# Performance work log

Hardware: AMD Instinct MI355X
Metric: run time of the kernel (lower is better)

The kernel has to match this reference:

```python
import jax, jax.numpy as jnp
import numpy as np

# HeteNet distribute_compute reference: per-agent expert id (hete_pick) selects one of
# E heterogeneous expert MLPs; tokens are gathered per expert, run through that expert's
# actor net, and scattered back into a padded [n_threads, n_agents, n_action] output.
# Here each expert is a 2-layer MLP (Net._act actor head approximation):
#   logits = relu(x @ W1[e] + b1[e]) @ W2[e] + b2[e]
# The dispatch/combine is expressed as dense per-expert compute + one-hot combine,
# which is the mathematically identical (mask-select) form of the gather/scatter.

T, N, D, H, A, E = 64, 64, 512, 512, 32, 15  # threads, agents, obs_dim(+addon), hidden, actions, experts


def setup_inputs() -> dict:
    key = jax.random.key(0)
    k0, k1, k2, k3 = jax.random.split(key, 4)
    obs = jax.random.normal(k0, (T, N, D), dtype=jnp.float32)
    hete_pick = jax.random.randint(k1, (T, N), 0, E)  # expert id per agent
    W1 = jax.random.normal(k2, (E, D, H), dtype=jnp.float32) * (1.0 / np.sqrt(D))
    b1 = jnp.zeros((E, H), dtype=jnp.float32)
    W2 = jax.random.normal(k3, (E, H, A), dtype=jnp.float32) * (1.0 / np.sqrt(H))
    b2 = jnp.zeros((E, A), dtype=jnp.float32)
    return {"obs": obs, "W1": W1, "b1": b1, "W2": W2, "b2": b2, "hete_pick": hete_pick}


def reference(obs, W1, b1, W2, b2, hete_pick):
    # per-expert dense forward: [E, T, N, H]
    h = jax.nn.relu(jnp.einsum('tnd,edh->etnh', obs, W1) + b1[:, None, None, :])
    logits = jnp.einsum('etnh,eha->etna', h, W2) + b2[:, None, None, :]  # [E,T,N,A]
    # combine: scatter each expert's rows back per mask (hete_pick == e)
    onehot = (hete_pick[None, :, :] == jnp.arange(E)[:, None, None]).astype(obs.dtype)  # [E,T,N]
    return jnp.einsum('etna,etn->tna', logits, onehot)  # [T,N,A]
```

## Files before the change

kernel.cpp:

```cpp
#include <hip/hip_runtime.h>
#include <stdint.h>

#define NTOK 4096
#define DDIM 512
#define HDIM 512
#define ADIM 32
#define NEXP 15
#define TILE_M 64
#define GRID_M 160

typedef __attribute__((ext_vector_type(8))) short bf16x8;
typedef __attribute__((ext_vector_type(8))) unsigned short ushort8;
typedef __attribute__((ext_vector_type(4))) unsigned short ushort4v;
typedef __attribute__((ext_vector_type(4))) float f32x4;

__device__ __forceinline__ unsigned short f2bf(float f) {
  unsigned int u = __float_as_uint(f);
  u += 0x7fffu + ((u >> 16) & 1u);
  return (unsigned short)(u >> 16);
}

__device__ __forceinline__ void gld_lds16(const void* g, void* l) {
  __builtin_amdgcn_global_load_lds(
      (const __attribute__((address_space(1))) void*)g,
      (__attribute__((address_space(3))) void*)l, 16, 0, 0);
}

__global__ __launch_bounds__(256) void prep_kernel(
    const float* __restrict__ W1, const float* __restrict__ W2,
    const int* __restrict__ pick, int* __restrict__ meta,
    int* __restrict__ lists, unsigned short* __restrict__ W1I,
    unsigned short* __restrict__ W2T, float* __restrict__ out)
{
  extern __shared__ char smem[];
  const int bid = blockIdx.x;
  const int tid = threadIdx.x;
  if (bid < 240) {
    float* s = (float*)smem;
    const int e = bid / 16, kc = bid % 16, r0 = kc * 32;
    const float* src = W1 + (size_t)e * (DDIM * HDIM) + (size_t)r0 * HDIM;
    #pragma unroll
    for (int v = 0; v < 16; ++v) {
      int i = v * 256 + tid;
      int row = i >> 7, col = (i & 127) * 4;
      *(float4*)(s + row * 517 + col) = *(const float4*)(src + (size_t)row * 512 + col);
    }
    __syncthreads();
    unsigned short* dst = W1I + (size_t)(e * 16 + kc) * 512 * 32;
    const int p = tid & 3;
    #pragma unroll
    for (int w = 0; w < 8; ++w) {
      int n = w * 64 + (tid >> 2);
      int q = p ^ ((n >> 1) & 3);
      ushort8 vv;
      #pragma unroll
      for (int x = 0; x < 8; ++x) vv[x] = f2bf(s[(q * 8 + x) * 517 + n]);
      *(ushort8*)(dst + (size_t)n * 32 + p * 8) = vv;
    }
  } else if (bid < 255) {
    float4 z4; z4.x = 0.f; z4.y = 0.f; z4.z = 0.f; z4.w = 0.f;
    for (int i = (bid - 240) * 256 + tid; i < NTOK * ADIM / 4; i += 15 * 256)
      ((float4*)out)[i] = z4;
    float* s = (float*)smem;
    const int e = bid - 240;
    const float* src = W2 + (size_t)e * (HDIM * ADIM);
    #pragma unroll
    for (int v = 0; v < 16; ++v) {
      int i = v * 256 + tid;
      int row = i >> 3, col = (i & 7) * 4;
      *(float4*)(s + row * 36 + col) = *(const float4*)(src + (size_t)row * 32 + col);
    }
    __syncthreads();
    unsigned short* dst = W2T + (size_t)e * (ADIM * HDIM);
    const int a = tid >> 3, k0 = (tid & 7) * 64;
    #pragma unroll
    for (int w = 0; w < 8; ++w) {
      ushort8 vv;
      #pragma unroll
      for (int x = 0; x < 8; ++x) vv[x] = f2bf(s[(size_t)(k0 + w * 8 + x) * 36 + a]);
      *(ushort8*)(dst + (size_t)a * 512 + k0 + w * 8) = vv;
    }
  } else {
    int* s_inc = (int*)smem;
    int* s_run = s_inc + NEXP * 256;
    int pk[16];
    #pragma unroll
    for (int i = 0; i < 16; ++i) pk[i] = pick[tid * 16 + i];
    #pragma unroll
    for (int e = 0; e < NEXP; ++e) {
      int c = 0;
      #pragma unroll
      for (int i = 0; i < 16; ++i) c += (pk[i] == e) ? 1 : 0;
      s_inc[e * 256 + tid] = c;
    }
    __syncthreads();
    for (int off = 1; off < 256; off <<= 1) {
      int v[NEXP];
      #pragma unroll
      for (int e = 0; e < NEXP; ++e) v[e] = (tid >= off) ? s_inc[e * 256 + tid - off] : 0;
      __syncthreads();
      #pragma unroll
      for (int e = 0; e < NEXP; ++e) s_inc[e * 256 + tid] += v[e];
      __syncthreads();
    }
    #pragma unroll
    for (int e = 0; e < NEXP; ++e) s_run[e * 256 + tid] = (tid > 0) ? s_inc[e * 256 + tid - 1] : 0;
    __syncthreads();
    #pragma unroll
    for (int i = 0; i < 16; ++i) {
      int p = pk[i];
      int pos = s_run[p * 256 + tid]++;
      lists[p * NTOK + pos] = tid * 16 + i;
    }
    if (tid < NEXP) meta[tid] = s_inc[tid * 256 + 255];
    __syncthreads();
    if (tid == 0) {
      int tot = 0;
      for (int ee = 0; ee < NEXP; ++ee) {
        int c = s_inc[ee * 256 + 255];
        int nt = (c + TILE_M - 1) / TILE_M;
        for (int i = 0; i < nt; ++i) meta[16 + tot++] = (ee << 16) | i;
      }
      meta[15] = tot;
    }
  }
}

__global__ __launch_bounds__(256, 1) void moe_gemm(
    const float* __restrict__ obs, const float* __restrict__ b1,
    const float* __restrict__ b2, const int* __restrict__ meta,
    const int* __restrict__ lists, const unsigned short* __restrict__ W1I,
    const unsigned short* __restrict__ W2T, float* __restrict__ out)
{
  const int ntiles = meta[15];
  const int nphys = ntiles * 2;
  const int p = blockIdx.x;
  const int xq = nphys >> 3, xr = nphys & 7;
  const int xcd = p & 7, slot = p >> 3;
  const int cx = xq + (xcd < xr ? 1 : 0);
  if (slot >= cx) return;
  const int j2 = xcd * xq + (xcd < xr ? xcd : xr) + slot;
  const int jt = j2 >> 1, half = j2 & 1;

  const int tl = meta[16 + jt];
  const int e = tl >> 16;
  const int tile_lo = (tl & 0xffff) * TILE_M;
  const int cnt = meta[e];
  int mvalid = cnt - tile_lo; if (mvalid > TILE_M) mvalid = TILE_M;

  extern __shared__ char smem[];
  char* s_x = smem;
  char* wb0 = smem + 65536;
  char* wb1 = smem + 81920;
  char* wb2 = smem + 98304;

  const int tid = threadIdx.x, lane = tid & 63, wave = tid >> 6;
  const int l15 = lane & 15, l4 = lane >> 4;
  const int nbl = wave * 64;
  const int hbase = half * 256;
  const int* mylist = lists + e * NTOK;
  const unsigned short* w1i_e = W1I + (size_t)e * 16 * 512 * 32;
  const unsigned short* w2t_e = W2T + (size_t)e * (ADIM * HDIM);

  auto issue_w1 = [&](int t, char* buf) {
    const unsigned short* base = w1i_e + (size_t)t * (512 * 32) + (size_t)hbase * 32;
    #pragma unroll
    for (int i = 0; i < 4; ++i) {
      int nb = nbl + i * 16;
      gld_lds16(base + (size_t)nb * 32 + lane * 8, buf + nb * 64);
    }
  };
  issue_w1(0, wb0);
  __builtin_amdgcn_sched_barrier(0);
  issue_w1(1, wb1);
  __builtin_amdgcn_sched_barrier(0);

  {
    const int m = tid >> 2, sq = tid & 3;
    int idx = tile_lo + m; if (idx >= cnt) idx = cnt - 1;
    const float* grow = obs + (size_t)mylist[idx] * DDIM;
    #pragma unroll 4
    for (int si = 0; si < 16; ++si) {
      const int s = sq + si * 4;
      float4 f0 = *(const float4*)(grow + s * 8);
      float4 f1 = *(const float4*)(grow + s * 8 + 4);
      ushort8 v;
      v[0] = f2bf(f0.x); v[1] = f2bf(f0.y); v[2] = f2bf(f0.z); v[3] = f2bf(f0.w);
      v[4] = f2bf(f1.x); v[5] = f2bf(f1.y); v[6] = f2bf(f1.z); v[7] = f2bf(f1.w);
      *(ushort8*)(s_x + m * 1024 + ((s ^ (m & 7)) << 4)) = v;
    }
  }
  __syncthreads();

  f32x4 acc[4][4];
  #pragma unroll
  for (int nt = 0; nt < 4; ++nt) {
    float4 bv = *(const float4*)(b1 + e * HDIM + hbase + nbl + nt * 16 + l4 * 4);
    f32x4 b4 = {bv.x, bv.y, bv.z, bv.w};
    #pragma unroll
    for (int mt = 0; mt < 4; ++mt) acc[nt][mt] = b4;
  }

  #pragma unroll
  for (int t = 0; t < 16; ++t) {
    if (t < 14) {
      char* nxt = ((t + 2) % 3 == 0) ? wb0 : ((t + 2) % 3 == 1) ? wb1 : wb2;
      issue_w1(t + 2, nxt);
    } else if (t == 14) {
      #pragma unroll
      for (int i = 0; i < 4; ++i) {
        int o = wave * 4096 + i * 1024 + lane * 16;
        int a = o >> 9;
        int p16 = (o >> 4) & 31;
        gld_lds16(w2t_e + (size_t)a * 512 + hbase + (size_t)((p16 ^ (a & 7)) * 8),
                  wb1 + o);
      }
    }
    if (t < 15) asm volatile("s_waitcnt vmcnt(8)" ::: "memory");
    else        asm volatile("s_waitcnt vmcnt(4)" ::: "memory");
    __builtin_amdgcn_sched_barrier(0);

    const char* cw = (t % 3 == 0) ? wb0 : (t % 3 == 1) ? wb1 : wb2;
    bf16x8 wfr[4], xfr[4];
    #pragma unroll
    for (int nt = 0; nt < 4; ++nt) {
      int n = nbl + nt * 16 + l15;
      wfr[nt] = *(const bf16x8*)(cw + n * 64 + ((l4 ^ ((n >> 1) & 3)) << 4));
    }
    #pragma unroll
    for (int mt = 0; mt < 4; ++mt) {
      int mm = mt * 16 + l15;
      xfr[mt] = *(const bf16x8*)(s_x + mm * 1024 + ((((t << 2) + l4) ^ (mm & 7)) << 4));
    }
    #pragma unroll
    for (int nt = 0; nt < 4; ++nt)
      #pragma unroll
      for (int mt = 0; mt < 4; ++mt)
        acc[nt][mt] = __builtin_amdgcn_mfma_f32_16x16x32_bf16(wfr[nt], xfr[mt], acc[nt][mt], 0, 0, 0);
  }

  __syncthreads();

  #pragma unroll
  for (int nt = 0; nt < 4; ++nt) {
    int n0 = nbl + nt * 16 + l4 * 4;
    int sg = n0 >> 3, hsel = (n0 >> 2) & 1;
    #pragma unroll
    for (int mt = 0; mt < 4; ++mt) {
      int mm = mt * 16 + l15;
      ushort4v hv;
      #pragma unroll
      for (int r = 0; r < 4; ++r) hv[r] = f2bf(fmaxf(acc[nt][mt][r], 0.f));
      *(ushort4v*)(s_x + mm * 1024 + ((sg ^ (mm & 7)) << 4) + hsel * 8) = hv;
    }
  }
  __syncthreads();

  const int mm2 = wave * 16 + l15;
  f32x4 acc2[2];
  #pragma unroll
  for (int at = 0; at < 2; ++at) {
    float b2v = half ? 0.f : b2[e * ADIM + at * 16 + l15];
    f32x4 b4 = {b2v, b2v, b2v, b2v};
    acc2[at] = b4;
  }
  #pragma unroll
  for (int ks = 0; ks < 8; ++ks) {
    bf16x8 af = *(const bf16x8*)(s_x + mm2 * 1024 + ((((ks << 2) + l4) ^ (mm2 & 7)) << 4));
    #pragma unroll
    for (int at = 0; at < 2; ++at) {
      int a = at * 16 + l15;
      bf16x8 bf = *(const bf16x8*)(wb1 + a * 512 + ((((ks << 2) + l4) ^ (a & 7)) << 4));
      acc2[at] = __builtin_amdgcn_mfma_f32_16x16x32_bf16(af, bf, acc2[at], 0, 0, 0);
    }
  }
  #pragma unroll
  for (int at = 0; at < 2; ++at)
    #pragma unroll
    for (int r = 0; r < 4; ++r) {
      int mrow = wave * 16 + l4 * 4 + r;
      if (mrow < mvalid)
        atomicAdd(&out[(size_t)mylist[tile_lo + mrow] * ADIM + at * 16 + l15], acc2[at][r]);
    }
}

__global__ __launch_bounds__(256) void naive_kernel(
    const float* __restrict__ obs, const float* __restrict__ W1,
    const float* __restrict__ b1, const float* __restrict__ W2,
    const float* __restrict__ b2, const int* __restrict__ pick,
    float* __restrict__ out)
{
  __shared__ float sx[DDIM];
  __shared__ float sh[HDIM];
  const int t = blockIdx.x, tid = threadIdx.x;
  const int e = pick[t];
  const float* x = obs + (size_t)t * DDIM;
  for (int i = tid; i < DDIM; i += 256) sx[i] = x[i];
  __syncthreads();
  const float* w1 = W1 + (size_t)e * DDIM * HDIM;
  for (int j = tid; j < HDIM; j += 256) {
    float a = b1[e * HDIM + j];
    for (int d = 0; d < DDIM; ++d) a = fmaf(sx[d], w1[(size_t)d * HDIM + j], a);
    sh[j] = a > 0.f ? a : 0.f;
  }
  __syncthreads();
  if (tid < ADIM) {
    const float* w2 = W2 + (size_t)e * HDIM * ADIM;
    float a = b2[e * ADIM + tid];
    for (int j = 0; j < HDIM; ++j) a = fmaf(sh[j], w2[(size_t)j * ADIM + tid], a);
    out[(size_t)t * ADIM + tid] = a;
  }
}

extern "C" void kernel_launch(void* const* d_in, const int* in_sizes, int n_in,
                              void* d_out, int out_size, void* d_ws, size_t ws_size,
                              hipStream_t stream)
{
  const float* obs = (const float*)d_in[0];
  const float* W1  = (const float*)d_in[1];
  const float* b1  = (const float*)d_in[2];
  const float* W2  = (const float*)d_in[3];
  const float* b2  = (const float*)d_in[4];
  const int* pick  = (const int*)d_in[5];
  float* out = (float*)d_out;
  (void)in_sizes; (void)n_in; (void)out_size;

  const size_t OFF_LISTS = 1024;
  const size_t OFF_W1I   = 262144;
  const size_t OFF_W2T   = OFF_W1I + (size_t)NEXP * HDIM * DDIM * 2;
  const size_t WS_NEEDED = OFF_W2T + (size_t)NEXP * ADIM * HDIM * 2;

  if (ws_size < WS_NEEDED) {
    naive_kernel<<<dim3(NTOK), dim3(256), 0, stream>>>(obs, W1, b1, W2, b2, pick, out);
    return;
  }

  char* ws = (char*)d_ws;
  int* meta   = (int*)ws;
  int* lists  = (int*)(ws + OFF_LISTS);
  unsigned short* W1I = (unsigned short*)(ws + OFF_W1I);
  unsigned short* W2T = (unsigned short*)(ws + OFF_W2T);

  prep_kernel<<<dim3(256), dim3(256), 73728, stream>>>(
      W1, W2, pick, meta, lists, W1I, W2T, out);
  moe_gemm<<<dim3(GRID_M), dim3(256), 114688, stream>>>(
      obs, b1, b2, meta, lists, W1I, W2T, out);
}
```

Baseline: 28.57 us.

## Halve MoE token tile to 32 rows, raise occupancy, prefetch obs early

Shrinks the per-expert token tile from 64 to 32 rows, which roughly doubles the number of tiles and the grid size. It cuts shared memory so two blocks can share a CU, and loads the obs rows into registers before issuing the W1 prefetch so the two transfers overlap. The second GEMM is remapped so each wave handles one 16x16 output block. The cost is that every expert weight block is streamed twice as often, raising weight traffic, while padding waste in partially filled tiles goes down.

```diff
diff --git a/kernel.cpp b/kernel.cpp
--- a/kernel.cpp
+++ b/kernel.cpp
@@ -6,8 +6,8 @@
 #define HDIM 512
 #define ADIM 32
 #define NEXP 15
-#define TILE_M 64
-#define GRID_M 160
+#define TILE_M 32
+#define GRID_M 288
 
 typedef __attribute__((ext_vector_type(8))) short bf16x8;
 typedef __attribute__((ext_vector_type(8))) unsigned short ushort8;
@@ -126,7 +126,7 @@
   }
 }
 
-__global__ __launch_bounds__(256, 1) void moe_gemm(
+__global__ __launch_bounds__(256, 2) void moe_gemm(
     const float* __restrict__ obs, const float* __restrict__ b1,
     const float* __restrict__ b2, const int* __restrict__ meta,
     const int* __restrict__ lists, const unsigned short* __restrict__ W1I,
@@ -150,9 +150,9 @@
 
   extern __shared__ char smem[];
   char* s_x = smem;
-  char* wb0 = smem + 65536;
-  char* wb1 = smem + 81920;
-  char* wb2 = smem + 98304;
+  char* wb0 = smem + 32768;
+  char* wb1 = smem + 49152;
+  char* wb2 = smem + 65536;
 
   const int tid = threadIdx.x, lane = tid & 63, wave = tid >> 6;
   const int l15 = lane & 15, l4 = lane >> 4;
@@ -162,6 +162,17 @@
   const unsigned short* w1i_e = W1I + (size_t)e * 16 * 512 * 32;
   const unsigned short* w2t_e = W2T + (size_t)e * (ADIM * HDIM);
 
+  const int m = tid >> 3, s8 = tid & 7;
+  int idx = tile_lo + m; if (idx >= cnt) idx = cnt - 1;
+  const float* grow = obs + (size_t)mylist[idx] * DDIM;
+  float4 xf[16];
+  #pragma unroll
+  for (int si = 0; si < 8; ++si) {
+    xf[si * 2]     = *(const float4*)(grow + (s8 + si * 8) * 8);
+    xf[si * 2 + 1] = *(const float4*)(grow + (s8 + si * 8) * 8 + 4);
+  }
+  __builtin_amdgcn_sched_barrier(0);
+
   auto issue_w1 = [&](int t, char* buf) {
     const unsigned short* base = w1i_e + (size_t)t * (512 * 32) + (size_t)hbase * 32;
     #pragma unroll
@@ -175,30 +186,23 @@
   issue_w1(1, wb1);
   __builtin_amdgcn_sched_barrier(0);
 
-  {
-    const int m = tid >> 2, sq = tid & 3;
-    int idx = tile_lo + m; if (idx >= cnt) idx = cnt - 1;
-    const float* grow = obs + (size_t)mylist[idx] * DDIM;
-    #pragma unroll 4
-    for (int si = 0; si < 16; ++si) {
-      const int s = sq + si * 4;
-      float4 f0 = *(const float4*)(grow + s * 8);
-      float4 f1 = *(const float4*)(grow + s * 8 + 4);
-      ushort8 v;
-      v[0] = f2bf(f0.x); v[1] = f2bf(f0.y); v[2] = f2bf(f0.z); v[3] = f2bf(f0.w);
-      v[4] = f2bf(f1.x); v[5] = f2bf(f1.y); v[6] = f2bf(f1.z); v[7] = f2bf(f1.w);
-      *(ushort8*)(s_x + m * 1024 + ((s ^ (m & 7)) << 4)) = v;
-    }
-  }
-  __syncthreads();
-
-  f32x4 acc[4][4];
+  #pragma unroll
+  for (int si = 0; si < 8; ++si) {
+    int s = s8 + si * 8;
+    float4 f0 = xf[si * 2], f1 = xf[si * 2 + 1];
+    ushort8 v;
+    v[0] = f2bf(f0.x); v[1] = f2bf(f0.y); v[2] = f2bf(f0.z); v[3] = f2bf(f0.w);
+    v[4] = f2bf(f1.x); v[5] = f2bf(f1.y); v[6] = f2bf(f1.z); v[7] = f2bf(f1.w);
+    *(ushort8*)(s_x + m * 1024 + ((s ^ (m & 7)) << 4)) = v;
+  }
+  __syncthreads();
+
+  f32x4 acc[4][2];
   #pragma unroll
   for (int nt = 0; nt < 4; ++nt) {
     float4 bv = *(const float4*)(b1 + e * HDIM + hbase + nbl + nt * 16 + l4 * 4);
     f32x4 b4 = {bv.x, bv.y, bv.z, bv.w};
-    #pragma unroll
-    for (int mt = 0; mt < 4; ++mt) acc[nt][mt] = b4;
+    acc[nt][0] = b4; acc[nt][1] = b4;
   }
 
   #pragma unroll
@@ -221,21 +225,21 @@
     __builtin_amdgcn_sched_barrier(0);
 
     const char* cw = (t % 3 == 0) ? wb0 : (t % 3 == 1) ? wb1 : wb2;
-    bf16x8 wfr[4], xfr[4];
+    bf16x8 wfr[4], xfr[2];
     #pragma unroll
     for (int nt = 0; nt < 4; ++nt) {
       int n = nbl + nt * 16 + l15;
       wfr[nt] = *(const bf16x8*)(cw + n * 64 + ((l4 ^ ((n >> 1) & 3)) << 4));
     }
     #pragma unroll
-    for (int mt = 0; mt < 4; ++mt) {
+    for (int mt = 0; mt < 2; ++mt) {
       int mm = mt * 16 + l15;
       xfr[mt] = *(const bf16x8*)(s_x + mm * 1024 + ((((t << 2) + l4) ^ (mm & 7)) << 4));
     }
     #pragma unroll
     for (int nt = 0; nt < 4; ++nt)
       #pragma unroll
-      for (int mt = 0; mt < 4; ++mt)
+      for (int mt = 0; mt < 2; ++mt)
         acc[nt][mt] = __builtin_amdgcn_mfma_f32_16x16x32_bf16(wfr[nt], xfr[mt], acc[nt][mt], 0, 0, 0);
   }
 
@@ -246,7 +250,7 @@
     int n0 = nbl + nt * 16 + l4 * 4;
     int sg = n0 >> 3, hsel = (n0 >> 2) & 1;
     #pragma unroll
-    for (int mt = 0; mt < 4; ++mt) {
+    for (int mt = 0; mt < 2; ++mt) {
       int mm = mt * 16 + l15;
       ushort4v hv;
       #pragma unroll
@@ -256,32 +260,23 @@
   }
   __syncthreads();
 
-  const int mm2 = wave * 16 + l15;
-  f32x4 acc2[2];
-  #pragma unroll
-  for (int at = 0; at < 2; ++at) {
-    float b2v = half ? 0.f : b2[e * ADIM + at * 16 + l15];
-    f32x4 b4 = {b2v, b2v, b2v, b2v};
-    acc2[at] = b4;
-  }
+  const int mt2 = wave >> 1, at2 = wave & 1;
+  const int a2 = at2 * 16 + l15;
+  float b2v = half ? 0.f : b2[e * ADIM + a2];
+  f32x4 acc2 = {b2v, b2v, b2v, b2v};
   #pragma unroll
   for (int ks = 0; ks < 8; ++ks) {
-    bf16x8 af = *(const bf16x8*)(s_x + mm2 * 1024 + ((((ks << 2) + l4) ^ (mm2 & 7)) << 4));
-    #pragma unroll
-    for (int at = 0; at < 2; ++at) {
-      int a = at * 16 + l15;
-      bf16x8 bf = *(const bf16x8*)(wb1 + a * 512 + ((((ks << 2) + l4) ^ (a & 7)) << 4));
-      acc2[at] = __builtin_amdgcn_mfma_f32_16x16x32_bf16(af, bf, acc2[at], 0, 0, 0);
-    }
-  }
-  #pragma unroll
-  for (int at = 0; at < 2; ++at)
-    #pragma unroll
-    for (int r = 0; r < 4; ++r) {
-      int mrow = wave * 16 + l4 * 4 + r;
-      if (mrow < mvalid)
-        atomicAdd(&out[(size_t)mylist[tile_lo + mrow] * ADIM + at * 16 + l15], acc2[at][r]);
-    }
+    int mm = mt2 * 16 + l15;
+    bf16x8 af = *(const bf16x8*)(s_x + mm * 1024 + ((((ks << 2) + l4) ^ (mm & 7)) << 4));
+    bf16x8 bf = *(const bf16x8*)(wb1 + a2 * 512 + ((((ks << 2) + l4) ^ (a2 & 7)) << 4));
+    acc2 = __builtin_amdgcn_mfma_f32_16x16x32_bf16(af, bf, acc2, 0, 0, 0);
+  }
+  #pragma unroll
+  for (int r = 0; r < 4; ++r) {
+    int mrow = mt2 * 16 + l4 * 4 + r;
+    if (mrow < mvalid)
+      atomicAdd(&out[(size_t)mylist[tile_lo + mrow] * ADIM + a2], acc2[r]);
+  }
 }
 
 __global__ __launch_bounds__(256) void naive_kernel(
@@ -343,6 +338,6 @@
 
   prep_kernel<<<dim3(256), dim3(256), 73728, stream>>>(
       W1, W2, pick, meta, lists, W1I, W2T, out);
-  moe_gemm<<<dim3(GRID_M), dim3(256), 114688, stream>>>(
+  moe_gemm<<<dim3(GRID_M), dim3(256), 81920, stream>>>(
       obs, b1, b2, meta, lists, W1I, W2T, out);
 }
```

Result: no change. 28.45 us (-0.4%).
